# Performance work log

Hardware: AMD Instinct MI355X
Metric: run time of the kernel (lower is better)

Reference implementation:

```python
import jax, jax.numpy as jnp
import numpy as np

DIM = 100

def setup_inputs() -> dict:
    key = jax.random.key(0)
    k1, k2, k3, k4, k5, k6 = jax.random.split(key, 6)
    n_items, B, L = 50000, 1024, 200
    item_embedding = jax.random.normal(k1, (n_items, DIM), dtype=jnp.float32)
    items = jax.random.randint(k2, (B, L), 0, n_items, dtype=jnp.int64)
    A = jax.random.uniform(k3, (B, B), dtype=jnp.float32)
    D = jax.random.uniform(k4, (B, B), dtype=jnp.float32)
    session_len = jax.random.uniform(k5, (B, 1), minval=1.0, maxval=float(L), dtype=jnp.float32)
    target_embedding = jax.random.normal(k6, (B, DIM), dtype=jnp.float32)
    return {"item_embedding": item_embedding, "items": items, "A": A, "D": D,
            "session_len": session_len, "target_embedding": target_embedding}

def reference(item_embedding, items, A, D, session_len, target_embedding):
    # Prepend a zero row (padding index 0 in the original torch code)
    emb = jnp.concatenate([jnp.zeros((1, item_embedding.shape[1]), item_embedding.dtype),
                           item_embedding], axis=0)          # [n+1, dim]
    seq_h = emb[items]                                        # [B, L, dim] gather
    rel = jnp.sum(seq_h, axis=1) / session_len                # [B, dim] mean-pool
    DA = jnp.matmul(D, A)                                     # [B, B]
    rel = jnp.matmul(DA, rel)                                 # [B, dim] propagation
    c = jax.nn.selu(rel)                                      # [B, dim]
    l_c = c / jnp.linalg.norm(c, axis=-1, keepdims=True)      # L2 normalize rows
    return l_c
```

## Files before the change

### kernel.cpp

```cpp
#include <hip/hip_runtime.h>
#include <math.h>

#define B_   1024
#define L_   200
#define DIM_ 100
#define NP   128
#define K_   1024
#define NCH  8

__global__ __launch_bounds__(512) void gather_pool_k(
    const float* __restrict__ emb, const int* __restrict__ items,
    const float* __restrict__ slen, float* __restrict__ relP) {
  const int b = blockIdx.x;
  const int t = threadIdx.x;
  const int s = t >> 7;
  const int d = t & 127;
  const int* __restrict__ row = items + b * L_ + s * (L_ / 4);
  float acc0 = 0.f, acc1 = 0.f;
  if (d < DIM_) {
    #pragma unroll
    for (int j = 0; j < L_ / 4; j += 2) {
      const int i0 = row[j];
      const int i1 = row[j + 1];
      if (i0 > 0) acc0 += emb[(size_t)(i0 - 1) * DIM_ + d];
      if (i1 > 0) acc1 += emb[(size_t)(i1 - 1) * DIM_ + d];
    }
  }
  __shared__ float sm[4][128];
  sm[s][d] = acc0 + acc1;
  __syncthreads();
  if (s == 0) {
    const float tot = sm[0][d] + sm[1][d] + sm[2][d] + sm[3][d];
    relP[b * NP + d] = (d < DIM_) ? tot / slen[b] : 0.f;
  }
}

#define BM 32
#define KT 16
__global__ __launch_bounds__(256) void gemm_splitk_k(
    const float* __restrict__ A,
    const float* __restrict__ Bm,
    float* __restrict__ Cpart) {
  __shared__ float As[BM][KT];
  __shared__ float Bs[KT][NP];
  const int t   = threadIdx.x;
  const int m0  = blockIdx.x * BM;
  const int k0b = blockIdx.y * (K_ / NCH);
  const int tc  = t & 31;
  const int tr  = t >> 5;
  float acc[4][4] = {};

  for (int k0 = k0b; k0 < k0b + K_ / NCH; k0 += KT) {
    if (t < 128) {
      const int r = t >> 2, kk = (t & 3) * 4;
      *(float4*)&As[r][kk] = *(const float4*)&A[(size_t)(m0 + r) * K_ + (k0 + kk)];
    }
    {
      const int e = t * 4;
      *(float4*)&Bs[e >> 7][e & 127] = *(const float4*)&Bm[(size_t)(k0 + (e >> 7)) * NP + (e & 127)];
      const int e2 = e + 1024;
      *(float4*)&Bs[e2 >> 7][e2 & 127] = *(const float4*)&Bm[(size_t)(k0 + (e2 >> 7)) * NP + (e2 & 127)];
    }
    __syncthreads();

    #pragma unroll
    for (int kk4 = 0; kk4 < KT; kk4 += 4) {
      float a[4][4], bb[4][4];
      #pragma unroll
      for (int i = 0; i < 4; ++i)
        *(float4*)a[i] = *(const float4*)&As[tr * 4 + i][kk4];
      #pragma unroll
      for (int j = 0; j < 4; ++j)
        *(float4*)bb[j] = *(const float4*)&Bs[kk4 + j][tc * 4];
      #pragma unroll
      for (int j = 0; j < 4; ++j)
        #pragma unroll
        for (int i = 0; i < 4; ++i)
          #pragma unroll
          for (int c = 0; c < 4; ++c)
            acc[i][c] += a[i][j] * bb[j][c];
    }
    __syncthreads();
  }

  float* Cc = Cpart + (size_t)blockIdx.y * B_ * NP;
  #pragma unroll
  for (int i = 0; i < 4; ++i)
    *(float4*)&Cc[(size_t)(m0 + tr * 4 + i) * NP + tc * 4] = *(float4*)acc[i];
}

__global__ __launch_bounds__(256) void reduce8_k(
    const float* __restrict__ part, float* __restrict__ outm) {
  const int i4 = blockIdx.x * 256 + threadIdx.x;
  const float4* p = (const float4*)part;
  float4 v = p[i4];
  #pragma unroll
  for (int c = 1; c < NCH; ++c) {
    float4 w = p[(size_t)c * (B_ * NP / 4) + i4];
    v.x += w.x; v.y += w.y; v.z += w.z; v.w += w.w;
  }
  ((float4*)outm)[i4] = v;
}

__global__ __launch_bounds__(128) void epilogue_k(
    const float* __restrict__ prePart, float* __restrict__ out) {
  const int b = blockIdx.x, c = threadIdx.x;
  float x = 0.f;
  #pragma unroll
  for (int p = 0; p < NCH; ++p)
    x += prePart[(size_t)p * B_ * NP + b * NP + c];
  const float scale = 1.0507009873554804934f;
  const float alpha = 1.6732632423543772848f;
  float s = (x > 0.f) ? (scale * x) : (scale * alpha * expm1f(x));
  if (c >= DIM_) s = 0.f;
  float ss = s * s;
  #pragma unroll
  for (int off = 32; off > 0; off >>= 1) ss += __shfl_down(ss, off, 64);
  __shared__ float wsum[2];
  if ((c & 63) == 0) wsum[c >> 6] = ss;
  __syncthreads();
  const float inv = 1.f / sqrtf(wsum[0] + wsum[1]);
  if (c < DIM_) out[b * DIM_ + c] = s * inv;
}

extern "C" void kernel_launch(void* const* d_in, const int* in_sizes, int n_in,
                              void* d_out, int out_size, void* d_ws, size_t ws_size,
                              hipStream_t stream) {
  const float* emb   = (const float*)d_in[0];
  const int*   items = (const int*)d_in[1];
  const float* A     = (const float*)d_in[2];
  const float* D     = (const float*)d_in[3];
  const float* slen  = (const float*)d_in[4];
  float* out = (float*)d_out;

  char* ws = (char*)d_ws;
  const size_t matB = (size_t)B_ * NP * sizeof(float);
  float* relP    = (float*)(ws);
  float* tPart   = (float*)(ws + 1 * matB);
  float* tM      = (float*)(ws + 9 * matB);
  float* prePart = (float*)(ws + 10 * matB);

  gather_pool_k<<<B_, 512, 0, stream>>>(emb, items, slen, relP);
  gemm_splitk_k<<<dim3(B_ / BM, NCH), 256, 0, stream>>>(A, relP, tPart);
  reduce8_k<<<B_ * NP / 4 / 256, 256, 0, stream>>>(tPart, tM);
  gemm_splitk_k<<<dim3(B_ / BM, NCH), 256, 0, stream>>>(D, tM, prePart);
  epilogue_k<<<B_, 128, 0, stream>>>(prePart, out);
}
```

Baseline: 123.8 us.

## Vectorize embedding gather with float4 and load whole K-chunk per GEMM block

The gather-pool kernel now reads each embedding row with float4 loads, using 8 groups of 25 active lanes that stride over the sequence, and reduces the groups through a shared-memory tree. The split-K GEMM doubles the chunk count to 16 and loads each block's full 64-wide K slice into shared memory once, removing the inner tile loop and its per-tile barriers. The aim is fewer load instructions, fewer synchronisations and more blocks for the GEMM. In exchange, the reduce and epilogue kernels must sum twice as many partial buffers, which adds memory traffic, and the workspace grows. The float4 embedding loads rely on 16-byte alignment, which holds because the row stride of 100 floats is a multiple of 4.

```diff
diff --git a/kernel.cpp b/kernel.cpp
--- a/kernel.cpp
+++ b/kernel.cpp
@@ -6,81 +6,95 @@
 #define DIM_ 100
 #define NP   128
 #define K_   1024
-#define NCH  8
+#define NCH  16
+#define KCH  (K_ / NCH)
 
-__global__ __launch_bounds__(512) void gather_pool_k(
+__global__ __launch_bounds__(256) void gather_pool_k(
     const float* __restrict__ emb, const int* __restrict__ items,
-    const float* __restrict__ slen, float* __restrict__ relP) {
+    const float* __restrict__ slen, float4* __restrict__ relP4) {
   const int b = blockIdx.x;
   const int t = threadIdx.x;
-  const int s = t >> 7;
-  const int d = t & 127;
-  const int* __restrict__ row = items + b * L_ + s * (L_ / 4);
-  float acc0 = 0.f, acc1 = 0.f;
-  if (d < DIM_) {
+  const int s = t >> 5;
+  const int c = t & 31;
+  const int* __restrict__ row = items + b * L_;
+  float4 acc = make_float4(0.f, 0.f, 0.f, 0.f);
+  if (c < 25) {
     #pragma unroll
-    for (int j = 0; j < L_ / 4; j += 2) {
-      const int i0 = row[j];
-      const int i1 = row[j + 1];
-      if (i0 > 0) acc0 += emb[(size_t)(i0 - 1) * DIM_ + d];
-      if (i1 > 0) acc1 += emb[(size_t)(i1 - 1) * DIM_ + d];
+    for (int j = 0; j < L_ / 8; ++j) {
+      const int idx = row[s + 8 * j];
+      if (idx > 0) {
+        const float4 v = *(const float4*)&emb[(size_t)(idx - 1) * DIM_ + c * 4];
+        acc.x += v.x; acc.y += v.y; acc.z += v.z; acc.w += v.w;
+      }
     }
   }
-  __shared__ float sm[4][128];
-  sm[s][d] = acc0 + acc1;
+  __shared__ float4 sm[8][32];
+  sm[s][c] = acc;
+  __syncthreads();
+  if (s < 4) {
+    float4 o = sm[s + 4][c];
+    sm[s][c].x += o.x; sm[s][c].y += o.y; sm[s][c].z += o.z; sm[s][c].w += o.w;
+  }
+  __syncthreads();
+  if (s < 2) {
+    float4 o = sm[s + 2][c];
+    sm[s][c].x += o.x; sm[s][c].y += o.y; sm[s][c].z += o.z; sm[s][c].w += o.w;
+  }
   __syncthreads();
   if (s == 0) {
-    const float tot = sm[0][d] + sm[1][d] + sm[2][d] + sm[3][d];
-    relP[b * NP + d] = (d < DIM_) ? tot / slen[b] : 0.f;
+    float4 a0 = sm[0][c], a1 = sm[1][c];
+    const float inv = 1.f / slen[b];
+    float4 r;
+    r.x = (a0.x + a1.x) * inv; r.y = (a0.y + a1.y) * inv;
+    r.z = (a0.z + a1.z) * inv; r.w = (a0.w + a1.w) * inv;
+    relP4[b * 32 + c] = (c < 25) ? r : make_float4(0.f, 0.f, 0.f, 0.f);
   }
 }
 
 #define BM 32
-#define KT 16
 __global__ __launch_bounds__(256) void gemm_splitk_k(
     const float* __restrict__ A,
     const float* __restrict__ Bm,
     float* __restrict__ Cpart) {
-  __shared__ float As[BM][KT];
-  __shared__ float Bs[KT][NP];
+  __shared__ float As[BM][KCH];
+  __shared__ float Bs[KCH][NP];
   const int t   = threadIdx.x;
   const int m0  = blockIdx.x * BM;
-  const int k0b = blockIdx.y * (K_ / NCH);
+  const int k0  = blockIdx.y * KCH;
   const int tc  = t & 31;
   const int tr  = t >> 5;
+
+  #pragma unroll
+  for (int q = 0; q < 2; ++q) {
+    const int f = t + q * 256;
+    const int r = f >> 4, kk = (f & 15) * 4;
+    *(float4*)&As[r][kk] = *(const float4*)&A[(size_t)(m0 + r) * K_ + (k0 + kk)];
+  }
+  #pragma unroll
+  for (int q = 0; q < 8; ++q) {
+    const int f = t + q * 256;
+    const int r = f >> 5, c = (f & 31) * 4;
+    *(float4*)&Bs[r][c] = *(const float4*)&Bm[(size_t)(k0 + r) * NP + c];
+  }
+  __syncthreads();
+
   float acc[4][4] = {};
-
-  for (int k0 = k0b; k0 < k0b + K_ / NCH; k0 += KT) {
-    if (t < 128) {
-      const int r = t >> 2, kk = (t & 3) * 4;
-      *(float4*)&As[r][kk] = *(const float4*)&A[(size_t)(m0 + r) * K_ + (k0 + kk)];
-    }
-    {
-      const int e = t * 4;
-      *(float4*)&Bs[e >> 7][e & 127] = *(const float4*)&Bm[(size_t)(k0 + (e >> 7)) * NP + (e & 127)];
-      const int e2 = e + 1024;
-      *(float4*)&Bs[e2 >> 7][e2 & 127] = *(const float4*)&Bm[(size_t)(k0 + (e2 >> 7)) * NP + (e2 & 127)];
-    }
-    __syncthreads();
-
+  #pragma unroll
+  for (int kk4 = 0; kk4 < KCH; kk4 += 4) {
+    float a[4][4], bb[4][4];
     #pragma unroll
-    for (int kk4 = 0; kk4 < KT; kk4 += 4) {
-      float a[4][4], bb[4][4];
+    for (int i = 0; i < 4; ++i)
+      *(float4*)a[i] = *(const float4*)&As[tr * 4 + i][kk4];
+    #pragma unroll
+    for (int j = 0; j < 4; ++j)
+      *(float4*)bb[j] = *(const float4*)&Bs[kk4 + j][tc * 4];
+    #pragma unroll
+    for (int j = 0; j < 4; ++j)
       #pragma unroll
       for (int i = 0; i < 4; ++i)
-        *(float4*)a[i] = *(const float4*)&As[tr * 4 + i][kk4];
-      #pragma unroll
-      for (int j = 0; j < 4; ++j)
-        *(float4*)bb[j] = *(const float4*)&Bs[kk4 + j][tc * 4];
-      #pragma unroll
-      for (int j = 0; j < 4; ++j)
         #pragma unroll
-        for (int i = 0; i < 4; ++i)
-          #pragma unroll
-          for (int c = 0; c < 4; ++c)
-            acc[i][c] += a[i][j] * bb[j][c];
-    }
-    __syncthreads();
+        for (int c = 0; c < 4; ++c)
+          acc[i][c] += a[i][j] * bb[j][c];
   }
 
   float* Cc = Cpart + (size_t)blockIdx.y * B_ * NP;
@@ -89,7 +103,7 @@
     *(float4*)&Cc[(size_t)(m0 + tr * 4 + i) * NP + tc * 4] = *(float4*)acc[i];
 }
 
-__global__ __launch_bounds__(256) void reduce8_k(
+__global__ __launch_bounds__(256) void reduce_k(
     const float* __restrict__ part, float* __restrict__ outm) {
   const int i4 = blockIdx.x * 256 + threadIdx.x;
   const float4* p = (const float4*)part;
@@ -137,12 +151,12 @@
   const size_t matB = (size_t)B_ * NP * sizeof(float);
   float* relP    = (float*)(ws);
   float* tPart   = (float*)(ws + 1 * matB);
-  float* tM      = (float*)(ws + 9 * matB);
-  float* prePart = (float*)(ws + 10 * matB);
+  float* tM      = (float*)(ws + 17 * matB);
+  float* prePart = (float*)(ws + 18 * matB);
 
-  gather_pool_k<<<B_, 512, 0, stream>>>(emb, items, slen, relP);
+  gather_pool_k<<<B_, 256, 0, stream>>>(emb, items, slen, (float4*)relP);
   gemm_splitk_k<<<dim3(B_ / BM, NCH), 256, 0, stream>>>(A, relP, tPart);
-  reduce8_k<<<B_ * NP / 4 / 256, 256, 0, stream>>>(tPart, tM);
+  reduce_k<<<B_ * NP / 4 / 256, 256, 0, stream>>>(tPart, tM);
   gemm_splitk_k<<<dim3(B_ / BM, NCH), 256, 0, stream>>>(D, tM, prePart);
   epilogue_k<<<B_, 128, 0, stream>>>(prePart, out);
 }
```

Result: faster. 110.2 us (-11.0%).
